# Kernel optimization log

Hardware: AMD Instinct MI355X
Metric: run time of the kernel (lower is better)

Reference implementation:

```python
import jax, jax.numpy as jnp
import numpy as np

N_SCALES = 3
BASE_SIGMA = 0.1
SCALES = jnp.asarray([BASE_SIGMA * 2.0 ** i for i in range(N_SCALES)], dtype=jnp.float32)


def setup_inputs() -> dict:
    key = jax.random.key(0)
    k_x, k_pos, k_tp, k_w1, k_b1, k_w2, k_b2 = jax.random.split(key, 7)
    B, C, T = 16, 306, 4000
    M = 128
    x = jax.random.normal(k_x, (B, C, T), dtype=jnp.float32)
    positions = jax.random.normal(k_pos, (B, C, 2), dtype=jnp.float32)
    target_positions = jax.random.normal(k_tp, (M, 2), dtype=jnp.float32)
    # nn.Linear(3, 32) / nn.Linear(32, 1) params (kaiming-uniform-ish init)
    lim1 = 1.0 / np.sqrt(3.0)
    w1 = jax.random.uniform(k_w1, (3, 32), jnp.float32, -lim1, lim1)
    b1 = jax.random.uniform(k_b1, (32,), jnp.float32, -lim1, lim1)
    lim2 = 1.0 / np.sqrt(32.0)
    w2 = jax.random.uniform(k_w2, (32, 1), jnp.float32, -lim2, lim2)
    b2 = jax.random.uniform(k_b2, (1,), jnp.float32, -lim2, lim2)
    return {"x": x, "positions": positions, "target_positions": target_positions,
            "w1": w1, "b1": b1, "w2": w2, "b2": b2}


def reference(x, positions, target_positions, w1, b1, w2, b2):
    # squared euclidean distances [B, C, M]
    diff = positions[:, :, None, :] - target_positions[None, None, :, :]
    d2 = jnp.sum(diff * diff, axis=-1)
    # multi-scale Gaussian kernels, stacked on last axis -> [B, C, M, n_scales]
    inv = 1.0 / (2.0 * SCALES ** 2)  # [n_scales]
    scale_weights = jnp.exp(-d2[..., None] * inv)
    # tiny 2-layer MLP gate: (3 -> 32 -> 1)
    h = jax.nn.relu(scale_weights @ w1 + b1)  # [B, C, M, 32]
    w = (h @ w2 + b2)[..., 0]                 # [B, C, M]
    # normalize over channel dim
    w = w / (jnp.sum(w, axis=1, keepdims=True) + 1e-8)
    # weighted channel aggregation -> [B, M, T]
    return jnp.einsum('bct,bcm->bmt', x, w)
```

## Files before the change

### kernel.cpp

```cpp
#include <hip/hip_runtime.h>

#define B_ 16
#define C_ 306
#define T_ 4000
#define M_ 128

typedef short bf16x8 __attribute__((ext_vector_type(8)));
typedef float f32x4 __attribute__((ext_vector_type(4)));

#define WF_PER_B 81920

__global__ __launch_bounds__(320)
void gate_kernel(const float* __restrict__ positions,
                 const float* __restrict__ target,
                 const float* __restrict__ w1,
                 const float* __restrict__ b1,
                 const float* __restrict__ w2,
                 const float* __restrict__ b2,
                 unsigned short* __restrict__ wf,
                 float* __restrict__ scale) {
    const int b  = blockIdx.x >> 5;
    const int mg = blockIdx.x & 31;
    const int tid = threadIdx.x;

    __shared__ float s_w1[96], s_b1[32], s_w2[32];
    __shared__ float s_b2;
    __shared__ float s_tgt[8];
    __shared__ float s_part[4][5];
    __shared__ unsigned short s_frag[40 * 72];

    if (tid < 96) s_w1[tid] = w1[tid];
    if (tid < 32) { s_b1[tid] = b1[tid]; s_w2[tid] = w2[tid]; }
    if (tid == 256) s_b2 = b2[0];
    if (tid >= 312) s_tgt[tid - 312] = target[mg * 8 + (tid - 312)];
    __syncthreads();

    float px = 0.0f, py = 0.0f;
    if (tid < C_) {
        px = positions[(b * C_ + tid) * 2 + 0];
        py = positions[(b * C_ + tid) * 2 + 1];
    }

    float wv_[4];
#pragma unroll
    for (int mi = 0; mi < 4; ++mi) {
        float w = 0.0f;
        if (tid < C_) {
            const float dx = px - s_tgt[mi * 2 + 0];
            const float dy = py - s_tgt[mi * 2 + 1];
            const float d2 = dx * dx + dy * dy;
            const float s2 = __expf(-d2 * 3.125f);
            const float q  = s2 * s2;
            const float s1 = q * q;
            const float r  = s1 * s1;
            const float s0 = r * r;
            float acc = s_b2;
#pragma unroll
            for (int j = 0; j < 32; ++j) {
                float h = fmaf(s0, s_w1[j],
                          fmaf(s1, s_w1[32 + j],
                          fmaf(s2, s_w1[64 + j], s_b1[j])));
                acc = fmaf(fmaxf(h, 0.0f), s_w2[j], acc);
            }
            w = acc;
        }
        wv_[mi] = w;
    }

#pragma unroll
    for (int mi = 0; mi < 4; ++mi) {
        float s = wv_[mi];
#pragma unroll
        for (int off = 32; off > 0; off >>= 1) s += __shfl_down(s, off, 64);
        if ((tid & 63) == 0) s_part[mi][tid >> 6] = s;
    }

    const int chunk = tid >> 3;
    const int slot  = tid & 7;
#pragma unroll
    for (int mi = 0; mi < 4; ++mi) {
        const float w = wv_[mi];
        const unsigned int u = __float_as_uint(w);
        const unsigned short h = (unsigned short)(u >> 16);
        const float lof = w - __uint_as_float(u & 0xffff0000u);
        const unsigned short l = (unsigned short)(__float_as_uint(lof) >> 16);
        s_frag[chunk * 72 + mi * 16 + 0 + slot] = h;
        s_frag[chunk * 72 + mi * 16 + 8 + slot] = l;
    }
    __syncthreads();

    if (tid < 4) {
        float tot = s_part[tid][0] + s_part[tid][1] + s_part[tid][2]
                  + s_part[tid][3] + s_part[tid][4];
        scale[b * M_ + mg * 4 + tid] = 1.0f / (tot + 1e-8f);
    }

    {
        const int ch = tid >> 3;
        const int g  = tid & 7;
        const uint4 v = *(const uint4*)(s_frag + ch * 72 + g * 8);
        unsigned short* dst = wf + (size_t)b * WF_PER_B
                            + (size_t)ch * 2048 + mg * 64 + g * 8;
        *(uint4*)dst = v;
    }
}

#define RS2 328

__global__ __launch_bounds__(256, 4)
void merge_gemm(const float* __restrict__ x,
                const unsigned short* __restrict__ wf,
                const float* __restrict__ scale,
                float* __restrict__ out) {
    const int t0 = blockIdx.x * 64;
    const int b  = blockIdx.y;
    const int tid  = threadIdx.x;
    const int lane = tid & 63;
    const int wv   = tid >> 6;
    const int tquad = lane >> 4;
    const int tsub  = lane & 15;

    __shared__ __align__(16) unsigned int sXh[2][4 * RS2];
    __shared__ __align__(16) unsigned int sXl[2][4 * RS2];
    __shared__ __align__(16) float sScale[M_];

    if (tid < M_) sScale[tid] = scale[b * M_ + tid];

    const float* xb = x + (size_t)b * C_ * T_;
    const unsigned short* wfB = wf + (size_t)b * WF_PER_B;

    f32x4 acc[4][2];
#pragma unroll
    for (int i = 0; i < 4; ++i)
#pragma unroll
        for (int j = 0; j < 2; ++j) acc[i][j] = (f32x4){0.f, 0.f, 0.f, 0.f};

    const int mw  = (wv & 1) * 64;
    const int tw2 = (wv >> 1) * 32;

    const int cp = tid >> 4;
    const int TQ = tid & 15;
    const float* xcol = xb + min(t0 + TQ * 4, T_ - 4);

    auto loadX = [&](int k, float4* xv) {
        const int c = k * 32 + 2 * cp;
        xv[0] = *(const float4*)(xcol + (size_t)min(c,     C_ - 1) * T_);
        xv[1] = *(const float4*)(xcol + (size_t)min(c + 1, C_ - 1) * T_);
    };
    auto loadW = [&](int k, bf16x8* ah_, bf16x8* al_) {
#pragma unroll
        for (int mi = 0; mi < 4; ++mi) {
            const size_t aoff = ((size_t)(k * 4 + tquad) * 128
                               + (mw + mi * 16 + tsub)) * 16;
            ah_[mi] = *(const bf16x8*)(wfB + aoff);
            al_[mi] = *(const bf16x8*)(wfB + aoff + 8);
        }
    };
    auto packX = [&](const float4* xv, unsigned int* Dh, unsigned int* Dl) {
        const int run = cp >> 2;
        const int pw  = cp & 3;
        const float* fa = (const float*)&xv[0];
        const float* fb = (const float*)&xv[1];
        const int base = run * RS2 + TQ * 20 + pw;
#pragma unroll
        for (int tt = 0; tt < 4; ++tt) {
            const unsigned int ua = __float_as_uint(fa[tt]);
            const unsigned int ub = __float_as_uint(fb[tt]);
            const float la = fa[tt] - __uint_as_float(ua & 0xffff0000u);
            const float lb = fb[tt] - __uint_as_float(ub & 0xffff0000u);
            Dh[base + tt * 4] = __builtin_amdgcn_perm(ub, ua, 0x07060302u);
            Dl[base + tt * 4] = __builtin_amdgcn_perm(__float_as_uint(lb),
                                                      __float_as_uint(la),
                                                      0x07060302u);
        }
    };

    bf16x8 ah[4], al[4];
    {
        float4 xv[2];
        loadX(0, xv);
        loadW(0, ah, al);
        packX(xv, &sXh[0][0], &sXl[0][0]);
    }
    asm volatile("s_waitcnt lgkmcnt(0)" ::: "memory");
    __builtin_amdgcn_s_barrier();
    asm volatile("" ::: "memory");

#pragma unroll
    for (int k = 0; k < 10; ++k) {
        float4 xn[2];
        if (k < 9) loadX(k + 1, xn);

        const unsigned int* Sh = &sXh[k & 1][0];
        const unsigned int* Sl = &sXl[k & 1][0];
        bf16x8 bh[2], bl[2];
#pragma unroll
        for (int i = 0; i < 2; ++i) {
            const int t = tw2 + i * 16 + tsub;
            const int a = tquad * RS2 + (t >> 2) * 20 + (t & 3) * 4;
            bh[i] = *(const bf16x8*)(Sh + a);
            bl[i] = *(const bf16x8*)(Sl + a);
        }

#pragma unroll
        for (int mi = 0; mi < 4; ++mi)
#pragma unroll
            for (int ti = 0; ti < 2; ++ti)
                acc[mi][ti] = __builtin_amdgcn_mfma_f32_16x16x32_bf16(
                    ah[mi], bh[ti], acc[mi][ti], 0, 0, 0);
#pragma unroll
        for (int mi = 0; mi < 4; ++mi)
#pragma unroll
            for (int ti = 0; ti < 2; ++ti)
                acc[mi][ti] = __builtin_amdgcn_mfma_f32_16x16x32_bf16(
                    ah[mi], bl[ti], acc[mi][ti], 0, 0, 0);
#pragma unroll
        for (int mi = 0; mi < 4; ++mi)
#pragma unroll
            for (int ti = 0; ti < 2; ++ti)
                acc[mi][ti] = __builtin_amdgcn_mfma_f32_16x16x32_bf16(
                    al[mi], bh[ti], acc[mi][ti], 0, 0, 0);

        if (k < 9) {
            loadW(k + 1, ah, al);
            packX(xn, &sXh[(k + 1) & 1][0], &sXl[(k + 1) & 1][0]);
            asm volatile("s_waitcnt lgkmcnt(0)" ::: "memory");
            __builtin_amdgcn_s_barrier();
            asm volatile("" ::: "memory");
        }
    }

#pragma unroll
    for (int mi = 0; mi < 4; ++mi) {
        const int mbase = mw + mi * 16 + tquad * 4;
        const float4 sc = *(const float4*)(sScale + mbase);
        float* op = out + ((size_t)b * M_ + mbase) * T_;
#pragma unroll
        for (int ti = 0; ti < 2; ++ti) {
            const int tg = t0 + tw2 + ti * 16 + tsub;
            if (tg < T_) {
                op[(size_t)0 * T_ + tg] = acc[mi][ti][0] * sc.x;
                op[(size_t)1 * T_ + tg] = acc[mi][ti][1] * sc.y;
                op[(size_t)2 * T_ + tg] = acc[mi][ti][2] * sc.z;
                op[(size_t)3 * T_ + tg] = acc[mi][ti][3] * sc.w;
            }
        }
    }
}

extern "C" void kernel_launch(void* const* d_in, const int* in_sizes, int n_in,
                              void* d_out, int out_size, void* d_ws, size_t ws_size,
                              hipStream_t stream) {
    const float* x         = (const float*)d_in[0];
    const float* positions = (const float*)d_in[1];
    const float* target    = (const float*)d_in[2];
    const float* w1        = (const float*)d_in[3];
    const float* b1        = (const float*)d_in[4];
    const float* w2        = (const float*)d_in[5];
    const float* b2        = (const float*)d_in[6];
    float* out = (float*)d_out;

    float* scale = (float*)d_ws;
    unsigned short* wf = (unsigned short*)(scale + B_ * M_);

    gate_kernel<<<B_ * 32, 320, 0, stream>>>(positions, target, w1, b1, w2, b2,
                                             wf, scale);

    dim3 grid((T_ + 63) / 64, B_);
    merge_gemm<<<grid, 256, 0, stream>>>(x, wf, scale, out);
}
```

Measured before the change: 154.9 us.

## Stage whole X tile in LDS upfront with swizzle, drop per-k barriers

The merge GEMM now loads all 10 channel chunks of its X tile at once (in two halves of five), splits them into bf16 hi/lo and stores them into a single XOR-swizzled LDS tile. The main MFMA loop then runs with no further barriers, and the scale vector is read straight from global memory. The aim is to issue many global loads at once and remove the nine per-iteration syncs. In exchange LDS use grows to about 80KB per block and launch bounds drop from 4 to 2 blocks per CU, so occupancy and latency hiding are reduced.

```diff
diff --git a/kernel.cpp b/kernel.cpp
--- a/kernel.cpp
+++ b/kernel.cpp
@@ -105,9 +105,9 @@
     }
 }
 
-#define RS2 328
-
-__global__ __launch_bounds__(256, 4)
+#define RS3 160
+
+__global__ __launch_bounds__(256, 2)
 void merge_gemm(const float* __restrict__ x,
                 const unsigned short* __restrict__ wf,
                 const float* __restrict__ scale,
@@ -120,33 +120,59 @@
     const int tquad = lane >> 4;
     const int tsub  = lane & 15;
 
-    __shared__ __align__(16) unsigned int sXh[2][4 * RS2];
-    __shared__ __align__(16) unsigned int sXl[2][4 * RS2];
-    __shared__ __align__(16) float sScale[M_];
-
-    if (tid < M_) sScale[tid] = scale[b * M_ + tid];
+    __shared__ __align__(16) unsigned int sX[2][64 * RS3];
 
     const float* xb = x + (size_t)b * C_ * T_;
     const unsigned short* wfB = wf + (size_t)b * WF_PER_B;
-
-    f32x4 acc[4][2];
-#pragma unroll
-    for (int i = 0; i < 4; ++i)
-#pragma unroll
-        for (int j = 0; j < 2; ++j) acc[i][j] = (f32x4){0.f, 0.f, 0.f, 0.f};
-
-    const int mw  = (wv & 1) * 64;
-    const int tw2 = (wv >> 1) * 32;
 
     const int cp = tid >> 4;
     const int TQ = tid & 15;
     const float* xcol = xb + min(t0 + TQ * 4, T_ - 4);
 
-    auto loadX = [&](int k, float4* xv) {
-        const int c = k * 32 + 2 * cp;
-        xv[0] = *(const float4*)(xcol + (size_t)min(c,     C_ - 1) * T_);
-        xv[1] = *(const float4*)(xcol + (size_t)min(c + 1, C_ - 1) * T_);
-    };
+#pragma unroll
+    for (int half = 0; half < 2; ++half) {
+        float4 va[5], vb[5];
+#pragma unroll
+        for (int j = 0; j < 5; ++j) {
+            const int k = half * 5 + j;
+            const int c = k * 32 + 2 * cp;
+            va[j] = *(const float4*)(xcol + (size_t)min(c,     C_ - 1) * T_);
+            vb[j] = *(const float4*)(xcol + (size_t)min(c + 1, C_ - 1) * T_);
+        }
+#pragma unroll
+        for (int j = 0; j < 5; ++j) {
+            const int k = half * 5 + j;
+            const int p = k * 16 + cp;
+            const float* fa = (const float*)&va[j];
+            const float* fb = (const float*)&vb[j];
+#pragma unroll
+            for (int tt = 0; tt < 4; ++tt) {
+                const int t = TQ * 4 + tt;
+                const int addr = t * RS3 + (p ^ ((t & 7) << 2));
+                const unsigned int ua = __float_as_uint(fa[tt]);
+                const unsigned int ub = __float_as_uint(fb[tt]);
+                const float la = fa[tt] - __uint_as_float(ua & 0xffff0000u);
+                const float lb = fb[tt] - __uint_as_float(ub & 0xffff0000u);
+                sX[0][addr] = __builtin_amdgcn_perm(ub, ua, 0x07060302u);
+                sX[1][addr] = __builtin_amdgcn_perm(__float_as_uint(lb),
+                                                    __float_as_uint(la),
+                                                    0x07060302u);
+            }
+        }
+    }
+    asm volatile("s_waitcnt lgkmcnt(0)" ::: "memory");
+    __builtin_amdgcn_s_barrier();
+    asm volatile("" ::: "memory");
+
+    f32x4 acc[4][2];
+#pragma unroll
+    for (int i = 0; i < 4; ++i)
+#pragma unroll
+        for (int j = 0; j < 2; ++j) acc[i][j] = (f32x4){0.f, 0.f, 0.f, 0.f};
+
+    const int mw  = (wv & 1) * 64;
+    const int tw2 = (wv >> 1) * 32;
+
     auto loadW = [&](int k, bf16x8* ah_, bf16x8* al_) {
 #pragma unroll
         for (int mi = 0; mi < 4; ++mi) {
@@ -156,50 +182,26 @@
             al_[mi] = *(const bf16x8*)(wfB + aoff + 8);
         }
     };
-    auto packX = [&](const float4* xv, unsigned int* Dh, unsigned int* Dl) {
-        const int run = cp >> 2;
-        const int pw  = cp & 3;
-        const float* fa = (const float*)&xv[0];
-        const float* fb = (const float*)&xv[1];
-        const int base = run * RS2 + TQ * 20 + pw;
-#pragma unroll
-        for (int tt = 0; tt < 4; ++tt) {
-            const unsigned int ua = __float_as_uint(fa[tt]);
-            const unsigned int ub = __float_as_uint(fb[tt]);
-            const float la = fa[tt] - __uint_as_float(ua & 0xffff0000u);
-            const float lb = fb[tt] - __uint_as_float(ub & 0xffff0000u);
-            Dh[base + tt * 4] = __builtin_amdgcn_perm(ub, ua, 0x07060302u);
-            Dl[base + tt * 4] = __builtin_amdgcn_perm(__float_as_uint(lb),
-                                                      __float_as_uint(la),
-                                                      0x07060302u);
-        }
-    };
+
+    int rbase[2], tswz[2];
+#pragma unroll
+    for (int ti = 0; ti < 2; ++ti) {
+        const int t = tw2 + ti * 16 + tsub;
+        rbase[ti] = t * RS3;
+        tswz[ti]  = (t & 7) << 2;
+    }
 
     bf16x8 ah[4], al[4];
-    {
-        float4 xv[2];
-        loadX(0, xv);
-        loadW(0, ah, al);
-        packX(xv, &sXh[0][0], &sXl[0][0]);
-    }
-    asm volatile("s_waitcnt lgkmcnt(0)" ::: "memory");
-    __builtin_amdgcn_s_barrier();
-    asm volatile("" ::: "memory");
+    loadW(0, ah, al);
 
 #pragma unroll
     for (int k = 0; k < 10; ++k) {
-        float4 xn[2];
-        if (k < 9) loadX(k + 1, xn);
-
-        const unsigned int* Sh = &sXh[k & 1][0];
-        const unsigned int* Sl = &sXl[k & 1][0];
         bf16x8 bh[2], bl[2];
 #pragma unroll
-        for (int i = 0; i < 2; ++i) {
-            const int t = tw2 + i * 16 + tsub;
-            const int a = tquad * RS2 + (t >> 2) * 20 + (t & 3) * 4;
-            bh[i] = *(const bf16x8*)(Sh + a);
-            bl[i] = *(const bf16x8*)(Sl + a);
+        for (int ti = 0; ti < 2; ++ti) {
+            const int q = rbase[ti] + ((k * 16 + tquad * 4) ^ tswz[ti]);
+            bh[ti] = *(const bf16x8*)(&sX[0][q]);
+            bl[ti] = *(const bf16x8*)(&sX[1][q]);
         }
 
 #pragma unroll
@@ -221,19 +223,13 @@
                 acc[mi][ti] = __builtin_amdgcn_mfma_f32_16x16x32_bf16(
                     al[mi], bh[ti], acc[mi][ti], 0, 0, 0);
 
-        if (k < 9) {
-            loadW(k + 1, ah, al);
-            packX(xn, &sXh[(k + 1) & 1][0], &sXl[(k + 1) & 1][0]);
-            asm volatile("s_waitcnt lgkmcnt(0)" ::: "memory");
-            __builtin_amdgcn_s_barrier();
-            asm volatile("" ::: "memory");
-        }
+        if (k < 9) loadW(k + 1, ah, al);
     }
 
 #pragma unroll
     for (int mi = 0; mi < 4; ++mi) {
         const int mbase = mw + mi * 16 + tquad * 4;
-        const float4 sc = *(const float4*)(sScale + mbase);
+        const float4 sc = *(const float4*)(scale + b * M_ + mbase);
         float* op = out + ((size_t)b * M_ + mbase) * T_;
 #pragma unroll
         for (int ti = 0; ti < 2; ++ti) {
```

New measurement: 153.5 us. Within noise of the previous version (-0.9%).
